# Performance work log

Hardware: AMD Instinct MI355X
Metric: run time of the kernel (lower is better)

Reference implementation:

```python
import jax, jax.numpy as jnp
import numpy as np

N_NODES = 100000
N_EDGES = 1600000
F_IN, F_HID, F_OUT = 15, 64, 64
N_MID = 6  # layers 1..6 of 8


def gcn_norm(edge_index, edge_weight, num_nodes):
    """PyG GCNConv normalization with self-loops (fill_value=1.0).
    Returns (src, dst, norm) over the augmented edge set."""
    src, dst = edge_index[0], edge_index[1]
    loop = jnp.arange(num_nodes)
    s = jnp.concatenate([src, loop])
    d = jnp.concatenate([dst, loop])
    w = jnp.concatenate([edge_weight, jnp.ones((num_nodes,), edge_weight.dtype)])
    deg = jax.ops.segment_sum(w, d, num_segments=num_nodes)
    dinv = jnp.where(deg > 0, jax.lax.rsqrt(deg), 0.0)
    norm = dinv[s] * w * dinv[d]  # [E+N]
    return s, d, norm


def gcn_layer(h, s, d, norm, W, b, num_nodes):
    h = h @ W                                  # dense transform [N, F_out]
    msg = norm[:, None] * h[s]                 # gather + scale   [E+N, F_out]
    out = jax.ops.segment_sum(msg, d, num_segments=num_nodes)  # scatter-add
    return out + b


def setup_inputs() -> dict:
    key = jax.random.key(0)
    ks = jax.random.split(key, 8)
    x = jax.random.normal(ks[0], (N_NODES, F_IN), jnp.float32)
    edge_index = jax.random.randint(ks[1], (2, N_EDGES), 0, N_NODES, jnp.int64)
    edge_weight = jax.random.uniform(ks[2], (N_EDGES,), jnp.float32)
    # glorot-ish scaling keeps activations sane through 8 layers
    W0 = jax.random.normal(ks[3], (F_IN, F_HID), jnp.float32) * (1.0 / np.sqrt(F_IN))
    b0 = jnp.zeros((F_HID,), jnp.float32)
    W_mid = jax.random.normal(ks[4], (N_MID, F_HID, F_HID), jnp.float32) * (1.0 / np.sqrt(F_HID))
    b_mid = jnp.zeros((N_MID, F_HID), jnp.float32)
    W_last = jax.random.normal(ks[5], (F_HID, F_OUT), jnp.float32) * (1.0 / np.sqrt(F_HID))
    b_last = jnp.zeros((F_OUT,), jnp.float32)
    return {"x": x, "edge_index": edge_index, "edge_weight": edge_weight,
            "W0": W0, "b0": b0, "W_mid": W_mid, "b_mid": b_mid,
            "W_last": W_last, "b_last": b_last}


def reference(x, edge_index, edge_weight, W0, b0, W_mid, b_mid, W_last, b_last):
    num_nodes = x.shape[0]
    s, d, norm = gcn_norm(edge_index, edge_weight, num_nodes)
    # layer 0
    h = gcn_layer(x, s, d, norm, W0, b0, num_nodes)
    h = jax.nn.relu(h)  # dropout is identity in eval mode
    # middle layers 1..6
    for i in range(N_MID):
        h = gcn_layer(h, s, d, norm, W_mid[i], b_mid[i], num_nodes)
        h = jax.nn.relu(h)
    # final layer + sigmoid
    h = gcn_layer(h, s, d, norm, W_last, b_last, num_nodes)
    return jax.nn.sigmoid(h)
```

## Files before the change

kernel.cpp:

```cpp
#include <hip/hip_runtime.h>
#include <hip/hip_fp16.h>
#include <math.h>

#define N_NODES 100000
#define N_EDGES 1600000
#define F_IN 15
#define MASK40 ((1ull << 40) - 1)

#define NBLK1 256
#define EPB   (N_EDGES / NBLK1)
#define NBUCK 256
#define NBUCK_USED ((N_NODES + 511) >> 9)

typedef _Float16 half8 __attribute__((ext_vector_type(8)));
typedef float f32x4 __attribute__((ext_vector_type(4)));


__global__ __launch_bounds__(1024) void k_hist(const int* __restrict__ dst,
                                               int* __restrict__ hist) {
    __shared__ int bins[NBUCK];
    int t = threadIdx.x, blk = blockIdx.x;
    if (t < NBUCK) bins[t] = 0;
    __syncthreads();
    int e0 = blk * EPB;
    for (int e = e0 + t; e < e0 + EPB; e += 1024)
        atomicAdd(&bins[dst[e] >> 9], 1);
    __syncthreads();
    if (t < NBUCK) hist[t * NBLK1 + blk] = bins[t];
}

__global__ __launch_bounds__(1024) void k_scan(int* __restrict__ hist,
                                               int* __restrict__ bucketBase,
                                               int* __restrict__ rowptr) {
    __shared__ int sc[1024];
    int t = threadIdx.x;
    int base = t * 64;
    int vals[64];
    int tot = 0;
#pragma unroll
    for (int k = 0; k < 64; k++) { vals[k] = hist[base + k]; tot += vals[k]; }
    sc[t] = tot;
    __syncthreads();
    for (int off = 1; off < 1024; off <<= 1) {
        int u = (t >= off) ? sc[t - off] : 0;
        __syncthreads();
        sc[t] += u;
        __syncthreads();
    }
    int run = sc[t] - tot;
#pragma unroll
    for (int k = 0; k < 64; k++) {
        int idx = base + k;
        if ((idx & (NBLK1 - 1)) == 0) bucketBase[idx / NBLK1] = run;
        int v = vals[k];
        hist[idx] = run;
        run += v;
    }
    if (t == 0) { bucketBase[NBUCK] = N_EDGES; rowptr[N_NODES] = N_EDGES; }
}

__global__ __launch_bounds__(1024) void k_scatter(const int* __restrict__ src,
        const int* __restrict__ dst, const float* __restrict__ w,
        const int* __restrict__ hist, int2* __restrict__ brec) {
    __shared__ int cursor[NBUCK];
    int t = threadIdx.x, blk = blockIdx.x;
    if (t < NBUCK) cursor[t] = hist[t * NBLK1 + blk];
    __syncthreads();
    int e0 = blk * EPB;
    for (int e = e0 + t; e < e0 + EPB; e += 1024) {
        int d = dst[e];
        int pos = atomicAdd(&cursor[d >> 9], 1);
        brec[pos] = make_int2(src[e] | ((d & 511) << 17), __float_as_int(w[e]));
    }
}

__global__ __launch_bounds__(512) void k_deg(const int2* __restrict__ brec,
        const int* __restrict__ bucketBase, float* __restrict__ dinv,
        int* __restrict__ rowptr) {
    __shared__ unsigned long long packedl[512];
    __shared__ int sc[512];
    int t = threadIdx.x, b = blockIdx.x;
    packedl[t] = 0ull;
    __syncthreads();
    int ebase = bucketBase[b], eend = bucketBase[b + 1];
    for (int e = ebase + t; e < eend; e += 512) {
        int2 r = brec[e];
        int dlo = (r.x >> 17) & 511;
        float wv = __int_as_float(r.y);
        unsigned long long contrib =
            (1ull << 40) + (unsigned long long)((double)wv * 4294967296.0);
        atomicAdd(&packedl[dlo], contrib);
    }
    __syncthreads();
    unsigned long long p = packedl[t];
    int cnt = (int)(p >> 40);
    int n = (b << 9) + t;
    if (n < N_NODES) {
        float deg = 1.0f + (float)((double)(p & MASK40) * 0x1p-32);
        dinv[n] = rsqrtf(deg);
    }
    sc[t] = cnt;
    __syncthreads();
    for (int off = 1; off < 512; off <<= 1) {
        int u = (t >= off) ? sc[t - off] : 0;
        __syncthreads();
        sc[t] += u;
        __syncthreads();
    }
    if (n < N_NODES) rowptr[n] = ebase + sc[t] - cnt;
}

__global__ __launch_bounds__(512) void k_csr(const int2* __restrict__ brec,
        const int* __restrict__ bucketBase, const int* __restrict__ rowptr,
        const float* __restrict__ dinv, int2* __restrict__ csr) {
    __shared__ int cursor[512];
    __shared__ float dl[512];
    int t = threadIdx.x, b = blockIdx.x;
    int n = (b << 9) + t;
    if (n < N_NODES) { cursor[t] = rowptr[n]; dl[t] = dinv[n]; }
    else             { cursor[t] = 0;         dl[t] = 0.f; }
    __syncthreads();
    int ebase = bucketBase[b], eend = bucketBase[b + 1];
    for (int e = ebase + t; e < eend; e += 512) {
        int2 r = brec[e];
        int dlo = (r.x >> 17) & 511;
        int s = r.x & 0x1FFFF;
        float wv = __int_as_float(r.y);
        int slot = atomicAdd(&cursor[dlo], 1);
        float nm = dinv[s] * wv * dl[dlo];
        csr[slot] = make_int2(s, __float_as_int(nm));
    }
}


__global__ void k_gemm0(const float* __restrict__ x, const float* __restrict__ W,
                        __half* __restrict__ out) {
    __shared__ float Ws[F_IN * 64];
    int t = threadIdx.x;
    for (int i = t; i < F_IN * 64; i += 256) Ws[i] = W[i];
    __syncthreads();
    int r = blockIdx.x * 4 + (t >> 6);
    int c = t & 63;
    if (r < N_NODES) {
        const float* xr = x + r * F_IN;
        float acc = 0.f;
#pragma unroll
        for (int k = 0; k < F_IN; k++) acc += xr[k] * Ws[k * 64 + c];
        out[r * 64 + c] = __float2half(acc);
    }
}


#define SE_CAP 128
#define G_STRIDE 72

template <bool WEP, bool SIG>
__global__ __launch_bounds__(256, 8) void k_gather4(
        const int* __restrict__ rowptr, const int2* __restrict__ csr,
        const __half* __restrict__ hin, const float* __restrict__ dinv,
        const float* __restrict__ W, const float* __restrict__ b,
        void* __restrict__ outp) {
    extern __shared__ char smem[];
    int t = threadIdx.x, wv = t >> 6, lane = t & 63;
    int sub = lane >> 5, fl = lane & 31;
    int2* se = (int2*)smem + wv * SE_CAP;
    _Float16* G = (_Float16*)(smem + 4 * SE_CAP * 8);

    int nb = blockIdx.x * 32;
    int n0w = nb + wv * 8;

    int rp[9];
#pragma unroll
    for (int j = 0; j < 9; j++) rp[j] = rowptr[n0w + j];
    int base = rp[0], end = rp[8];

    const __half2* h2 = (const __half2*)hin;

    float2 acc[8];
#pragma unroll
    for (int j = 0; j < 8; j++) {
        int n = n0w + j;
        float dv = dinv[n];
        __half2 hq = h2[n * 32 + fl];
        float w0 = (sub == 0) ? dv * dv : 0.f;
        acc[j].x = w0 * __low2float(hq);
        acc[j].y = w0 * __high2float(hq);
    }

    for (int cb = base; cb < end; cb += SE_CAP) {
        int ce = cb + SE_CAP; if (ce > end) ce = end;
        int cn = ce - cb;
        for (int i = lane; i < cn; i += 64) se[i] = csr[cb + i];
        __builtin_amdgcn_wave_barrier();
#pragma unroll
        for (int j = 0; j < 8; j++) {
            int lo = rp[j] < cb ? cb : rp[j];
            int hi = rp[j + 1] > ce ? ce : rp[j + 1];
            int i = lo - cb, iend = hi - cb;
            for (; i + 7 < iend; i += 8) {
                int2 r0 = se[i + sub],     r1 = se[i + 2 + sub];
                int2 r2 = se[i + 4 + sub], r3 = se[i + 6 + sub];
                __half2 q0 = h2[r0.x * 32 + fl];
                __half2 q1 = h2[r1.x * 32 + fl];
                __half2 q2 = h2[r2.x * 32 + fl];
                __half2 q3 = h2[r3.x * 32 + fl];
                float n0 = __int_as_float(r0.y), n1 = __int_as_float(r1.y);
                float n2 = __int_as_float(r2.y), n3 = __int_as_float(r3.y);
                acc[j].x = fmaf(n0, __low2float(q0), acc[j].x);
                acc[j].y = fmaf(n0, __high2float(q0), acc[j].y);
                acc[j].x = fmaf(n1, __low2float(q1), acc[j].x);
                acc[j].y = fmaf(n1, __high2float(q1), acc[j].y);
                acc[j].x = fmaf(n2, __low2float(q2), acc[j].x);
                acc[j].y = fmaf(n2, __high2float(q2), acc[j].y);
                acc[j].x = fmaf(n3, __low2float(q3), acc[j].x);
                acc[j].y = fmaf(n3, __high2float(q3), acc[j].y);
            }
            for (; i + 1 < iend; i += 2) {
                int2 r = se[i + sub];
                __half2 q = h2[r.x * 32 + fl];
                float nm = __int_as_float(r.y);
                acc[j].x = fmaf(nm, __low2float(q), acc[j].x);
                acc[j].y = fmaf(nm, __high2float(q), acc[j].y);
            }
            if (i < iend) {
                int2 r = se[i];
                __half2 q = h2[r.x * 32 + fl];
                float nm = (sub == 0) ? __int_as_float(r.y) : 0.f;
                acc[j].x = fmaf(nm, __low2float(q), acc[j].x);
                acc[j].y = fmaf(nm, __high2float(q), acc[j].y);
            }
        }
        __builtin_amdgcn_wave_barrier();
    }

#pragma unroll
    for (int j = 0; j < 8; j++) {
        acc[j].x += __shfl_xor(acc[j].x, 32);
        acc[j].y += __shfl_xor(acc[j].y, 32);
    }

    if (!WEP) {
        float2 bv = ((const float2*)b)[fl];
        if (sub == 0) {
#pragma unroll
            for (int j = 0; j < 8; j++) {
                float ox = fmaxf(acc[j].x + bv.x, 0.f);
                float oy = fmaxf(acc[j].y + bv.y, 0.f);
                ((__half2*)outp)[(n0w + j) * 32 + fl] = __floats2half2_rn(ox, oy);
            }
        }
        return;
    }

    if (sub == 0) {
        __half2* G2 = (__half2*)G;
#pragma unroll
        for (int j = 0; j < 8; j++)
            G2[(wv * 8 + j) * (G_STRIDE / 2) + fl] = __floats2half2_rn(acc[j].x, acc[j].y);
    }
    __syncthreads();

    int col = lane & 15, quad = lane >> 4;
    int mrow = (wv & 1) * 16;
    int nc0 = (wv >> 1) * 32;

    half8 af[2];
#pragma unroll
    for (int kt = 0; kt < 2; kt++)
        af[kt] = *(const half8*)&G[(mrow + col) * G_STRIDE + kt * 32 + quad * 8];

    __syncthreads();

    half8 bf[2][2][2];
#pragma unroll
    for (int nt = 0; nt < 2; nt++) {
#pragma unroll
        for (int kt = 0; kt < 2; kt++) {
#pragma unroll
            for (int j = 0; j < 8; j++) {
                float w = W[(kt * 32 + quad * 8 + j) * 64 + nc0 + nt * 16 + col];
                _Float16 hi = (_Float16)w;
                bf[nt][kt][0][j] = hi;
                bf[nt][kt][1][j] = (_Float16)(w - (float)hi);
            }
        }
    }

    f32x4 c0, c1;
    {
        float b0v = b[nc0 + col], b1v = b[nc0 + 16 + col];
        c0 = (f32x4){b0v, b0v, b0v, b0v};
        c1 = (f32x4){b1v, b1v, b1v, b1v};
    }
#pragma unroll
    for (int kt = 0; kt < 2; kt++) {
        c0 = __builtin_amdgcn_mfma_f32_16x16x32_f16(af[kt], bf[0][kt][0], c0, 0, 0, 0);
        c0 = __builtin_amdgcn_mfma_f32_16x16x32_f16(af[kt], bf[0][kt][1], c0, 0, 0, 0);
        c1 = __builtin_amdgcn_mfma_f32_16x16x32_f16(af[kt], bf[1][kt][0], c1, 0, 0, 0);
        c1 = __builtin_amdgcn_mfma_f32_16x16x32_f16(af[kt], bf[1][kt][1], c1, 0, 0, 0);
    }

    if (!SIG) {
#pragma unroll
        for (int nt = 0; nt < 2; nt++) {
            f32x4 c = nt ? c1 : c0;
#pragma unroll
            for (int r = 0; r < 4; r++) {
                float o = fmaxf(c[r], 0.f);
                G[(mrow + quad * 4 + r) * G_STRIDE + nc0 + nt * 16 + col] =
                    (_Float16)o;
            }
        }
        __syncthreads();
        {
            int row = t >> 3, seg = t & 7;
            half8 v = *(const half8*)&G[row * G_STRIDE + seg * 8];
            *(half8*)((__half*)outp + (nb + row) * 64 + seg * 8) = v;
        }
    } else {
        float* fo = (float*)smem;
#pragma unroll
        for (int nt = 0; nt < 2; nt++) {
            f32x4 c = nt ? c1 : c0;
#pragma unroll
            for (int r = 0; r < 4; r++) {
                float o = 1.0f / (1.0f + expf(-c[r]));
                fo[(mrow + quad * 4 + r) * 66 + nc0 + nt * 16 + col] = o;
            }
        }
        __syncthreads();
#pragma unroll
        for (int k = 0; k < 2; k++) {
            int lin = t + k * 256;
            int row = lin >> 4, seg = lin & 15;
            float4 v = *(const float4*)&fo[row * 66 + seg * 4];
            *(float4*)((float*)outp + (nb + row) * 64 + seg * 4) = v;
        }
    }
}


extern "C" void kernel_launch(void* const* d_in, const int* in_sizes, int n_in,
                              void* d_out, int out_size, void* d_ws, size_t ws_size,
                              hipStream_t stream) {
    const float* x  = (const float*)d_in[0];
    const int*   ei = (const int*)  d_in[1];
    const float* ew = (const float*)d_in[2];
    const float* W0 = (const float*)d_in[3];
    const float* b0 = (const float*)d_in[4];
    const float* Wm = (const float*)d_in[5];
    const float* bm = (const float*)d_in[6];
    const float* Wl = (const float*)d_in[7];
    const float* bl = (const float*)d_in[8];
    float* out = (float*)d_out;

    const int* src = ei;
    const int* dst = ei + N_EDGES;

    char* ws = (char*)d_ws;
    int*    hist   = (int*)  (ws + 0);
    int*    bbase  = (int*)  (ws + (1u << 18));
    float*  dinv   = (float*)(ws + (1u << 20));
    int*    rowptr = (int*)  (ws + (2u << 20));
    int2*   brec   = (int2*) (ws + (3u << 20));
    int2*   csr    = (int2*) (ws + (16u << 20));
    __half* htmp   = (__half*)(ws + (29u << 20));
    __half* hA     = (__half*)(ws + (42u << 20));
    __half* hB     = (__half*)(ws + (55u << 20));

    int gR4 = (N_NODES + 3) / 4;
    int gG  = N_NODES / 32;

    const size_t smem0 = 4 * SE_CAP * 8;
    const size_t smemW = 4 * SE_CAP * 8 + 32 * G_STRIDE * 2;

    hipLaunchKernelGGL(k_hist,    dim3(NBLK1), dim3(1024), 0, stream, dst, hist);
    hipLaunchKernelGGL(k_scan,    dim3(1),     dim3(1024), 0, stream, hist, bbase, rowptr);
    hipLaunchKernelGGL(k_scatter, dim3(NBLK1), dim3(1024), 0, stream, src, dst, ew, hist, brec);
    hipLaunchKernelGGL(k_deg,     dim3(NBUCK_USED), dim3(512), 0, stream, brec, bbase, dinv, rowptr);
    hipLaunchKernelGGL(k_csr,     dim3(NBUCK_USED), dim3(512), 0, stream, brec, bbase, rowptr, dinv, csr);

    hipLaunchKernelGGL(k_gemm0,   dim3(gR4), dim3(256), 0, stream, x, W0, htmp);
    hipLaunchKernelGGL((k_gather4<false, false>), dim3(gG), dim3(256), smem0, stream,
                       rowptr, csr, htmp, dinv, (const float*)nullptr, b0, (void*)hA);

    __half* hin = hA;
    __half* hout = hB;
    for (int i = 0; i < 6; i++) {
        const float* Wi = Wm + (long)i * 64 * 64;
        const float* bi = bm + (long)i * 64;
        hipLaunchKernelGGL((k_gather4<true, false>), dim3(gG), dim3(256), smemW, stream,
                           rowptr, csr, hin, dinv, Wi, bi, (void*)hout);
        __half* t2 = hin; hin = hout; hout = t2;
    }

    hipLaunchKernelGGL((k_gather4<true, true>), dim3(gG), dim3(256), smemW, stream,
                       rowptr, csr, hin, dinv, Wl, bl, (void*)out);
}
```

Before: 512.2 us.

## Process 48 nodes per block and restructure fused MFMA epilogue into row bands

Each gather block now handles 48 nodes (12 per wave) instead of 32, with bounds checks for the ragged tail. The fused 64x64 transform is reorganised so each wave owns a 16-column slice and loops over three 16-row bands. Results go to a separate staging buffer, which removes one block-wide barrier. The aim is to amortise W loading and hi/lo splitting over more rows and give each wave more gather work for latency hiding. The cost is higher register use from 12 accumulators and larger shared memory, which may reduce occupancy.

```diff
diff --git a/kernel.cpp b/kernel.cpp
--- a/kernel.cpp
+++ b/kernel.cpp
@@ -153,6 +153,9 @@
 
 #define SE_CAP 128
 #define G_STRIDE 72
+#define NPB 48
+#define NPW 12
+#define GG ((N_NODES + NPB - 1) / NPB)
 
 template <bool WEP, bool SIG>
 __global__ __launch_bounds__(256, 8) void k_gather4(
@@ -165,23 +168,29 @@
     int sub = lane >> 5, fl = lane & 31;
     int2* se = (int2*)smem + wv * SE_CAP;
     _Float16* G = (_Float16*)(smem + 4 * SE_CAP * 8);
-
-    int nb = blockIdx.x * 32;
-    int n0w = nb + wv * 8;
-
-    int rp[9];
-#pragma unroll
-    for (int j = 0; j < 9; j++) rp[j] = rowptr[n0w + j];
-    int base = rp[0], end = rp[8];
+    char* stg = smem + 4 * SE_CAP * 8 + NPB * G_STRIDE * 2;
+
+    int nb = blockIdx.x * NPB;
+    int n0w = nb + wv * NPW;
+
+    int rp[NPW + 1];
+#pragma unroll
+    for (int j = 0; j <= NPW; j++) {
+        int idx = n0w + j;
+        rp[j] = rowptr[idx < N_NODES ? idx : N_NODES];
+    }
+    int base = rp[0], end = rp[NPW];
 
     const __half2* h2 = (const __half2*)hin;
 
-    float2 acc[8];
-#pragma unroll
-    for (int j = 0; j < 8; j++) {
+    float2 acc[NPW];
+#pragma unroll
+    for (int j = 0; j < NPW; j++) {
         int n = n0w + j;
-        float dv = dinv[n];
-        __half2 hq = h2[n * 32 + fl];
+        bool valid = n < N_NODES;
+        float dv = valid ? dinv[n] : 0.f;
+        int nc = valid ? n : 0;
+        __half2 hq = h2[nc * 32 + fl];
         float w0 = (sub == 0) ? dv * dv : 0.f;
         acc[j].x = w0 * __low2float(hq);
         acc[j].y = w0 * __high2float(hq);
@@ -193,7 +202,7 @@
         for (int i = lane; i < cn; i += 64) se[i] = csr[cb + i];
         __builtin_amdgcn_wave_barrier();
 #pragma unroll
-        for (int j = 0; j < 8; j++) {
+        for (int j = 0; j < NPW; j++) {
             int lo = rp[j] < cb ? cb : rp[j];
             int hi = rp[j + 1] > ce ? ce : rp[j + 1];
             int i = lo - cb, iend = hi - cb;
@@ -234,7 +243,7 @@
     }
 
 #pragma unroll
-    for (int j = 0; j < 8; j++) {
+    for (int j = 0; j < NPW; j++) {
         acc[j].x += __shfl_xor(acc[j].x, 32);
         acc[j].y += __shfl_xor(acc[j].y, 32);
     }
@@ -243,10 +252,13 @@
         float2 bv = ((const float2*)b)[fl];
         if (sub == 0) {
 #pragma unroll
-            for (int j = 0; j < 8; j++) {
-                float ox = fmaxf(acc[j].x + bv.x, 0.f);
-                float oy = fmaxf(acc[j].y + bv.y, 0.f);
-                ((__half2*)outp)[(n0w + j) * 32 + fl] = __floats2half2_rn(ox, oy);
+            for (int j = 0; j < NPW; j++) {
+                int n = n0w + j;
+                if (n < N_NODES) {
+                    float ox = fmaxf(acc[j].x + bv.x, 0.f);
+                    float oy = fmaxf(acc[j].y + bv.y, 0.f);
+                    ((__half2*)outp)[n * 32 + fl] = __floats2half2_rn(ox, oy);
+                }
             }
         }
         return;
@@ -255,86 +267,76 @@
     if (sub == 0) {
         __half2* G2 = (__half2*)G;
 #pragma unroll
-        for (int j = 0; j < 8; j++)
-            G2[(wv * 8 + j) * (G_STRIDE / 2) + fl] = __floats2half2_rn(acc[j].x, acc[j].y);
+        for (int j = 0; j < NPW; j++)
+            G2[(wv * NPW + j) * (G_STRIDE / 2) + fl] = __floats2half2_rn(acc[j].x, acc[j].y);
     }
     __syncthreads();
 
     int col = lane & 15, quad = lane >> 4;
-    int mrow = (wv & 1) * 16;
-    int nc0 = (wv >> 1) * 32;
-
-    half8 af[2];
-#pragma unroll
-    for (int kt = 0; kt < 2; kt++)
-        af[kt] = *(const half8*)&G[(mrow + col) * G_STRIDE + kt * 32 + quad * 8];
-
-    __syncthreads();
-
-    half8 bf[2][2][2];
-#pragma unroll
-    for (int nt = 0; nt < 2; nt++) {
-#pragma unroll
-        for (int kt = 0; kt < 2; kt++) {
-#pragma unroll
-            for (int j = 0; j < 8; j++) {
-                float w = W[(kt * 32 + quad * 8 + j) * 64 + nc0 + nt * 16 + col];
-                _Float16 hi = (_Float16)w;
-                bf[nt][kt][0][j] = hi;
-                bf[nt][kt][1][j] = (_Float16)(w - (float)hi);
-            }
-        }
-    }
-
-    f32x4 c0, c1;
-    {
-        float b0v = b[nc0 + col], b1v = b[nc0 + 16 + col];
-        c0 = (f32x4){b0v, b0v, b0v, b0v};
-        c1 = (f32x4){b1v, b1v, b1v, b1v};
-    }
+    int nc0 = wv * 16;
+
+    half8 bf[2][2];
 #pragma unroll
     for (int kt = 0; kt < 2; kt++) {
-        c0 = __builtin_amdgcn_mfma_f32_16x16x32_f16(af[kt], bf[0][kt][0], c0, 0, 0, 0);
-        c0 = __builtin_amdgcn_mfma_f32_16x16x32_f16(af[kt], bf[0][kt][1], c0, 0, 0, 0);
-        c1 = __builtin_amdgcn_mfma_f32_16x16x32_f16(af[kt], bf[1][kt][0], c1, 0, 0, 0);
-        c1 = __builtin_amdgcn_mfma_f32_16x16x32_f16(af[kt], bf[1][kt][1], c1, 0, 0, 0);
-    }
+#pragma unroll
+        for (int j = 0; j < 8; j++) {
+            float w = W[(kt * 32 + quad * 8 + j) * 64 + nc0 + col];
+            _Float16 hi = (_Float16)w;
+            bf[kt][0][j] = hi;
+            bf[kt][1][j] = (_Float16)(w - (float)hi);
+        }
+    }
+    float b0v = b[nc0 + col];
+
+#pragma unroll
+    for (int band = 0; band < 3; band++) {
+        half8 a0 = *(const half8*)&G[(band * 16 + col) * G_STRIDE + 0 * 32 + quad * 8];
+        half8 a1 = *(const half8*)&G[(band * 16 + col) * G_STRIDE + 1 * 32 + quad * 8];
+        f32x4 c = (f32x4){b0v, b0v, b0v, b0v};
+        c = __builtin_amdgcn_mfma_f32_16x16x32_f16(a0, bf[0][0], c, 0, 0, 0);
+        c = __builtin_amdgcn_mfma_f32_16x16x32_f16(a0, bf[0][1], c, 0, 0, 0);
+        c = __builtin_amdgcn_mfma_f32_16x16x32_f16(a1, bf[1][0], c, 0, 0, 0);
+        c = __builtin_amdgcn_mfma_f32_16x16x32_f16(a1, bf[1][1], c, 0, 0, 0);
+
+        if (!SIG) {
+            _Float16* S = (_Float16*)stg;
+#pragma unroll
+            for (int r = 0; r < 4; r++)
+                S[(band * 16 + quad * 4 + r) * G_STRIDE + nc0 + col] =
+                    (_Float16)fmaxf(c[r], 0.f);
+        } else {
+            float* S = (float*)stg;
+#pragma unroll
+            for (int r = 0; r < 4; r++)
+                S[(band * 16 + quad * 4 + r) * 68 + nc0 + col] =
+                    1.0f / (1.0f + expf(-c[r]));
+        }
+    }
+    __syncthreads();
 
     if (!SIG) {
-#pragma unroll
-        for (int nt = 0; nt < 2; nt++) {
-            f32x4 c = nt ? c1 : c0;
-#pragma unroll
-            for (int r = 0; r < 4; r++) {
-                float o = fmaxf(c[r], 0.f);
-                G[(mrow + quad * 4 + r) * G_STRIDE + nc0 + nt * 16 + col] =
-                    (_Float16)o;
-            }
-        }
-        __syncthreads();
-        {
-            int row = t >> 3, seg = t & 7;
-            half8 v = *(const half8*)&G[row * G_STRIDE + seg * 8];
-            *(half8*)((__half*)outp + (nb + row) * 64 + seg * 8) = v;
-        }
-    } else {
-        float* fo = (float*)smem;
-#pragma unroll
-        for (int nt = 0; nt < 2; nt++) {
-            f32x4 c = nt ? c1 : c0;
-#pragma unroll
-            for (int r = 0; r < 4; r++) {
-                float o = 1.0f / (1.0f + expf(-c[r]));
-                fo[(mrow + quad * 4 + r) * 66 + nc0 + nt * 16 + col] = o;
-            }
-        }
-        __syncthreads();
+        const _Float16* S = (const _Float16*)stg;
 #pragma unroll
         for (int k = 0; k < 2; k++) {
             int lin = t + k * 256;
+            if (lin < 48 * 8) {
+                int row = lin >> 3, seg = lin & 7;
+                if (nb + row < N_NODES) {
+                    half8 v = *(const half8*)&S[row * G_STRIDE + seg * 8];
+                    *(half8*)((__half*)outp + (nb + row) * 64 + seg * 8) = v;
+                }
+            }
+        }
+    } else {
+        const float* S = (const float*)stg;
+#pragma unroll
+        for (int k = 0; k < 3; k++) {
+            int lin = t + k * 256;
             int row = lin >> 4, seg = lin & 15;
-            float4 v = *(const float4*)&fo[row * 66 + seg * 4];
-            *(float4*)((float*)outp + (nb + row) * 64 + seg * 4) = v;
+            if (nb + row < N_NODES) {
+                float4 v = *(const float4*)&S[row * 68 + seg * 4];
+                *(float4*)((float*)outp + (nb + row) * 64 + seg * 4) = v;
+            }
         }
     }
 }
@@ -369,10 +371,10 @@
     __half* hB     = (__half*)(ws + (55u << 20));
 
     int gR4 = (N_NODES + 3) / 4;
-    int gG  = N_NODES / 32;
 
     const size_t smem0 = 4 * SE_CAP * 8;
-    const size_t smemW = 4 * SE_CAP * 8 + 32 * G_STRIDE * 2;
+    const size_t smemM = 4 * SE_CAP * 8 + NPB * G_STRIDE * 2 * 2;
+    const size_t smemS = 4 * SE_CAP * 8 + NPB * G_STRIDE * 2 + NPB * 68 * 4;
 
     hipLaunchKernelGGL(k_hist,    dim3(NBLK1), dim3(1024), 0, stream, dst, hist);
     hipLaunchKernelGGL(k_scan,    dim3(1),     dim3(1024), 0, stream, hist, bbase, rowptr);
@@ -381,7 +383,7 @@
     hipLaunchKernelGGL(k_csr,     dim3(NBUCK_USED), dim3(512), 0, stream, brec, bbase, rowptr, dinv, csr);
 
     hipLaunchKernelGGL(k_gemm0,   dim3(gR4), dim3(256), 0, stream, x, W0, htmp);
-    hipLaunchKernelGGL((k_gather4<false, false>), dim3(gG), dim3(256), smem0, stream,
+    hipLaunchKernelGGL((k_gather4<false, false>), dim3(GG), dim3(256), smem0, stream,
                        rowptr, csr, htmp, dinv, (const float*)nullptr, b0, (void*)hA);
 
     __half* hin = hA;
@@ -389,11 +391,11 @@
     for (int i = 0; i < 6; i++) {
         const float* Wi = Wm + (long)i * 64 * 64;
         const float* bi = bm + (long)i * 64;
-        hipLaunchKernelGGL((k_gather4<true, false>), dim3(gG), dim3(256), smemW, stream,
+        hipLaunchKernelGGL((k_gather4<true, false>), dim3(GG), dim3(256), smemM, stream,
                            rowptr, csr, hin, dinv, Wi, bi, (void*)hout);
         __half* t2 = hin; hin = hout; hout = t2;
     }
 
-    hipLaunchKernelGGL((k_gather4<true, true>), dim3(gG), dim3(256), smemW, stream,
+    hipLaunchKernelGGL((k_gather4<true, true>), dim3(GG), dim3(256), smemS, stream,
                        rowptr, csr, hin, dinv, Wl, bl, (void*)out);
 }
```

New measurement: 600.8 us. 1.17x slower.
